# Optimization experiments

Hardware: AMD Instinct MI355X
Metric: run time of the kernel (lower is better)

The kernel has to match this reference:

```python
import jax, jax.numpy as jnp
import numpy as np
from jax import lax

NUM_HEADS = 8
NUM_LAYERS = 3


def _conv3d(x, w, b):
    # x: [B,C,D,H,W], w: [O,I,3,3,3] (torch Conv3d layout), padding=1, stride=1
    y = lax.conv_general_dilated(x, w, window_strides=(1, 1, 1),
                                 padding=[(1, 1)] * 3,
                                 dimension_numbers=('NCDHW', 'OIDHW', 'NCDHW'))
    return y + b[None, :, None, None, None]


def _attn(x, wq, bq, wk, bk, wv, bv, gamma):
    # Faithful translation of MultiHeadAttentionModule.forward
    B, C, D, H, W = x.shape
    N = D * H * W
    hd = C // NUM_HEADS
    scale = jnp.asarray(hd ** 0.5, x.dtype)
    xf = x.reshape(B, C, N).transpose(0, 2, 1)  # [B,N,C]

    def proj(wm, bm):
        # torch Linear: y = x @ W.T + b ; split C -> (heads, head_dim)
        return (xf @ wm.T + bm).reshape(B, N, NUM_HEADS, hd).transpose(0, 2, 1, 3)

    q = proj(wq, bq)  # [B,h,N,d]
    k = proj(wk, bk)
    v = proj(wv, bv)
    energy = jnp.einsum('bhnd,bhmd->bhnm', q, k) / scale  # [B,h,N,N]
    attn = jax.nn.softmax(energy, axis=-1)
    o = jnp.einsum('bhnm,bhmd->bhnd', attn, v)  # [B,h,N,d]
    # permute(0,1,3,2).view(in_shape): channel order is (head, head_dim)
    o = o.transpose(0, 1, 3, 2).reshape(B, C, D, H, W)
    return gamma * o + x


def setup_inputs() -> dict:
    key = jax.random.key(0)
    ks = jax.random.split(key, 16)
    B, Cin, D, H, W = 1, 64, 16, 16, 16
    Co = 128
    L = NUM_LAYERS
    s = 0.02
    return {
        'x': jax.random.normal(ks[0], (B, Cin, D, H, W), jnp.float32),
        'lateral_w': jax.random.normal(ks[1], (Co, Cin, 3, 3, 3), jnp.float32) * s,
        'lateral_b': jax.random.normal(ks[2], (Co,), jnp.float32) * s,
        'pos': jax.random.normal(ks[3], (1, Co, D, H, W), jnp.float32) * s,
        'qw': jax.random.normal(ks[4], (L, Co, Co), jnp.float32) * s,
        'qb': jax.random.normal(ks[5], (L, Co), jnp.float32) * s,
        'kw': jax.random.normal(ks[6], (L, Co, Co), jnp.float32) * s,
        'kb': jax.random.normal(ks[7], (L, Co), jnp.float32) * s,
        'vw': jax.random.normal(ks[8], (L, Co, Co), jnp.float32) * s,
        'vb': jax.random.normal(ks[9], (L, Co), jnp.float32) * s,
        'gamma': jnp.full((L,), 0.5, jnp.float32),
        'out_w': jax.random.normal(ks[10], (Co, Co, 3, 3, 3), jnp.float32) * s,  # ConvTranspose3d weight [in,out,k,k,k]
        'out_b': jax.random.normal(ks[11], (Co,), jnp.float32) * s,
    }


def reference(x, lateral_w, lateral_b, pos, qw, qb, kw, kb, vw, vb, gamma, out_w, out_b):
    # t_dim == 1 branch of FPN3DWithMultiHeadAttention.forward
    lat = _conv3d(x, lateral_w, lateral_b) + pos
    for i in range(NUM_LAYERS):
        lat = _attn(lat, qw[i], qb[i], kw[i], kb[i], vw[i], vb[i], gamma[i])
    # ConvTranspose3d(k=3, stride=1, pad=1) == Conv3d with spatially flipped,
    # channel-transposed kernel and padding k-1-p = 1
    w_eq = jnp.flip(out_w, axis=(2, 3, 4)).transpose(1, 0, 2, 3, 4)
    return _conv3d(lat, w_eq, out_b)
```

## Files before the change

### kernel.cpp

```cpp
#include <hip/hip_runtime.h>
#include <hip/hip_bf16.h>

#define NVOX 4096
#define CDIM 128

typedef __attribute__((ext_vector_type(8)))  short bf16x8;
typedef __attribute__((ext_vector_type(4)))  float f32x4;
typedef __attribute__((ext_vector_type(16))) float f32x16;

static __device__ __forceinline__ short f2bf(float f) {
    __hip_bfloat16 h = __float2bfloat16(f);
    union { __hip_bfloat16 h; short s; } u; u.h = h; return u.s;
}
static __device__ __forceinline__ float bf2f(short s) {
    union { unsigned u; float f; } u;
    u.u = ((unsigned)(unsigned short)s) << 16;
    return u.f;
}
static __device__ __forceinline__ float fexp2(float x) {
    return __builtin_amdgcn_exp2f(x);
}
__device__ __forceinline__ int permpos(int ci) {
    return (((ci >> 2) & 3) << 3) + (ci & 3) + ((ci & 16) >> 2) + ((ci >> 5) << 5);
}
__device__ __forceinline__ int invp(int p) {
    const int c = p >> 5, r = p & 31, g = (r >> 3) & 3, j = r & 7;
    return (c << 5) + (j < 4 ? (g << 2) + j : 16 + (g << 2) + (j - 4));
}
__device__ __forceinline__ int pos16(int d) {
    return (d & 3) | ((d & 4) << 1) | ((d & 8) >> 1);
}

__global__ __launch_bounds__(256) void pack_all(
    const float* __restrict__ x,  const float* __restrict__ lw,
    const float* __restrict__ qw, const float* __restrict__ kw, const float* __restrict__ vw,
    const float* __restrict__ ow,
    short* __restrict__ xp, short* __restrict__ wb1, short* __restrict__ wqkv, short* __restrict__ wb2,
    short* __restrict__ xp2)
{
    const int b = blockIdx.x;
    const int tid = threadIdx.x;
    if (b < 1458) {
        const int e = b * 256 + tid;
        if (e >= 5832 * 64) return;
        const int vp = e >> 6, p = e & 63;
        const int z = vp / 324, rem = vp - z * 324, y = rem / 18, xx = rem % 18;
        short val = 0;
        if (z >= 1 && z <= 16 && y >= 1 && y <= 16 && xx >= 1 && xx <= 16) {
            const int n = ((z - 1) * 16 + (y - 1)) * 16 + (xx - 1);
            val = f2bf(x[invp(p) * NVOX + n]);
        }
        xp[e] = val;
    } else if (b < 1458 + 864) {
        const int e = (b - 1458) * 256 + tid;
        if (e >= 27 * 128 * 64) return;
        const int t = e >> 13, co = (e >> 6) & 127, p = e & 63;
        wb1[e] = f2bf(lw[(co * 64 + invp(p)) * 27 + t]);
    } else if (b < 1458 + 864 + 576) {
        const int e = (b - 2322) * 256 + tid;
        if (e >= 3 * 3 * 128 * 128) return;
        const int l = e / 49152, r = e - l * 49152;
        const int m = r >> 14, co = (r >> 7) & 127, p = r & 127;
        const float* W = (m == 0 ? qw : m == 1 ? kw : vw) + l * 16384;
        wqkv[e] = f2bf(W[co * 128 + invp(p)]);
    } else if (b < 1458 + 864 + 576 + 1728) {
        const int e = (b - 2898) * 256 + tid;
        if (e >= 27 * 128 * 128) return;
        const int t = e >> 14, co = (e >> 7) & 127, p = e & 127;
        wb2[e] = f2bf(ow[(invp(p) * 128 + co) * 27 + (26 - t)]);
    } else {
        const int e = (b - 4626) * 256 + tid;
        if (e >= 5832 * 16) return;
        const int4 z4 = {0, 0, 0, 0};
        *reinterpret_cast<int4*>(xp2 + e * 8) = z4;
    }
}

__global__ __launch_bounds__(256) void conv1_mfma(
    const short* __restrict__ xp,
    const short* __restrict__ wb,
    const float* __restrict__ bias, const float* __restrict__ pos,
    short* __restrict__ latbf)
{
    __shared__ short bl[324 * 72];
    const int tid = threadIdx.x;
    const int g = blockIdx.x;
    const int cot = g >> 6;
    const int vgrp = g & 63;
    const int r0 = vgrp * 4;
    const int z = r0 >> 4, y0 = r0 & 15;

    for (int i = tid; i < 2592; i += 256) {
        const int col = i >> 3, pc = i & 7;
        const int line = col / 18, xq = col - line * 18;
        const int dz = line / 6, yi = line - dz * 6;
        const int4 v = *reinterpret_cast<const int4*>(
            xp + (((z + dz) * 18 + (y0 + yi)) * 18 + xq) * 64 + pc * 8);
        const int slot = ((((pc >> 2) ^ col) & 1) << 5) + ((pc & 3) << 3);
        *reinterpret_cast<int4*>(&bl[col * 72 + slot]) = v;
    }
    __syncthreads();

    const int wid = tid >> 6, lane = tid & 63;
    const int lg = lane >> 4, lq = lane & 15;
    const int wc = wid >> 1, wv = wid & 1;
    const int co0 = cot * 32 + wc * 16;

    const short* pA = wb + (co0 + lq) * 64 + lg * 8;

    auto ldA = [&](int t, bf16x8* A) {
        const short* p = pA + t * 8192;
        #pragma unroll
        for (int c = 0; c < 2; ++c) A[c] = *reinterpret_cast<const bf16x8*>(p + c * 32);
    };

    f32x4 acc0 = {0.f,0.f,0.f,0.f}, acc1 = {0.f,0.f,0.f,0.f};

    auto comp = [&](int t, const bf16x8* A) {
        const int dz = t / 9, r9 = t - dz * 9, dy = r9 / 3, dx = r9 - dy * 3;
        #pragma unroll
        for (int ry = 0; ry < 2; ++ry) {
            const int col = (dz * 6 + wv * 2 + ry + dy) * 18 + dx + lq;
            const short* bp = &bl[col * 72 + (lg << 3)];
            #pragma unroll
            for (int c = 0; c < 2; ++c) {
                const bf16x8 b = *reinterpret_cast<const bf16x8*>(bp + (((c ^ col) & 1) << 5));
                if (ry == 0) acc0 = __builtin_amdgcn_mfma_f32_16x16x32_bf16(A[c], b, acc0, 0, 0, 0);
                else         acc1 = __builtin_amdgcn_mfma_f32_16x16x32_bf16(A[c], b, acc1, 0, 0, 0);
            }
        }
    };

    bf16x8 A0[2], A1[2];
    int t = 0;
    ldA(0, A0);
    while (true) {
        if (t + 1 < 27) ldA(t + 1, A1);
        comp(t, A0);
        if (++t >= 27) break;
        if (t + 1 < 27) ldA(t + 1, A0);
        comp(t, A1);
        if (++t >= 27) break;
    }

    #pragma unroll
    for (int ry = 0; ry < 2; ++ry) {
        const f32x4 a = ry ? acc1 : acc0;
        const int n = (r0 + wv * 2 + ry) * 16 + lq;
        short4 s4;
        #pragma unroll
        for (int i = 0; i < 4; ++i) {
            const int co = co0 + 4 * lg + i;
            const float v = a[i] + bias[co] + pos[co * NVOX + n];
            ((short*)&s4)[i] = f2bf(v);
        }
        *reinterpret_cast<short4*>(latbf + n * 128 + permpos(co0 + 4 * lg)) = s4;
    }
}

__global__ __launch_bounds__(256) void proj_mfma(
    const short* __restrict__ latbf,
    const short* __restrict__ wl,
    const float* __restrict__ bq, const float* __restrict__ bk, const float* __restrict__ bv,
    short* __restrict__ qP, short* __restrict__ kP, short* __restrict__ vP)
{
    const int m = blockIdx.z;
    const int wid = threadIdx.x >> 6, lane = threadIdx.x & 63;
    const int lg = lane >> 4, lq = lane & 15;
    const int co0 = blockIdx.y * 16;
    const int row0 = (blockIdx.x * 4 + wid) * 2;

    const short* A = wl + m * 16384 + (co0 + lq) * 128 + lg * 8;
    bf16x8 Af[4];
    #pragma unroll
    for (int c = 0; c < 4; ++c) Af[c] = *reinterpret_cast<const bf16x8*>(A + c * 32);

    const short* Bp0 = latbf + (row0 * 16 + lq) * 128 + lg * 8;
    const short* Bp1 = Bp0 + 16 * 128;
    bf16x8 Bf0[4], Bf1[4];
    #pragma unroll
    for (int c = 0; c < 4; ++c) Bf0[c] = *reinterpret_cast<const bf16x8*>(Bp0 + c * 32);
    #pragma unroll
    for (int c = 0; c < 4; ++c) Bf1[c] = *reinterpret_cast<const bf16x8*>(Bp1 + c * 32);

    f32x4 a0a = {0.f,0.f,0.f,0.f}, a0b = a0a, a1a = a0a, a1b = a0a;
    a0a = __builtin_amdgcn_mfma_f32_16x16x32_bf16(Af[0], Bf0[0], a0a, 0, 0, 0);
    a1a = __builtin_amdgcn_mfma_f32_16x16x32_bf16(Af[0], Bf1[0], a1a, 0, 0, 0);
    a0b = __builtin_amdgcn_mfma_f32_16x16x32_bf16(Af[1], Bf0[1], a0b, 0, 0, 0);
    a1b = __builtin_amdgcn_mfma_f32_16x16x32_bf16(Af[1], Bf1[1], a1b, 0, 0, 0);
    a0a = __builtin_amdgcn_mfma_f32_16x16x32_bf16(Af[2], Bf0[2], a0a, 0, 0, 0);
    a1a = __builtin_amdgcn_mfma_f32_16x16x32_bf16(Af[2], Bf1[2], a1a, 0, 0, 0);
    a0b = __builtin_amdgcn_mfma_f32_16x16x32_bf16(Af[3], Bf0[3], a0b, 0, 0, 0);
    a1b = __builtin_amdgcn_mfma_f32_16x16x32_bf16(Af[3], Bf1[3], a1b, 0, 0, 0);

    const int h = blockIdx.y;
    #pragma unroll
    for (int rr = 0; rr < 2; ++rr) {
        const f32x4 acc = rr ? (a1a + a1b) : (a0a + a0b);
        const int row = row0 + rr;
        const int n = row * 16 + lq;
        if (m == 2) {
            const int col = row * 16 + pos16(lq);
            #pragma unroll
            for (int r = 0; r < 4; ++r) {
                const int d = lg * 4 + r;
                vP[(h * 17 + d) * NVOX + col] = f2bf(acc[r] + bv[co0 + d]);
            }
            if (lg == 0) vP[(h * 17 + 16) * NVOX + col] = (short)0x3F80;
        } else {
            const float* bias = (m == 0) ? bq : bk;
            const float S = (m == 0) ? 0.25f * 1.4426950408889634f : 1.f;
            const int pg = ((lg & 1) << 3) | ((lg & 2) << 1);
            short4 s4;
            #pragma unroll
            for (int r = 0; r < 4; ++r) {
                const int co = co0 + lg * 4 + r;
                ((short*)&s4)[r] = f2bf((acc[r] + bias[co]) * S);
            }
            short* dst = (m == 0) ? qP : kP;
            *reinterpret_cast<short4*>(dst + ((h << 12) + n) * 16 + pg) = s4;
        }
    }
}

__global__ __launch_bounds__(512) void attn_mfma(
    const short* __restrict__ qP, const short* __restrict__ kP, const short* __restrict__ vP,
    short* __restrict__ latbf, short* __restrict__ outbf,
    const float* __restrict__ gamma, int layer, int last)
{
    __shared__ float smO[8][64][17];
    const int tid = threadIdx.x;
    const int wid = tid >> 6, lane = tid & 63;
    const int l5 = lane >> 5, lm = lane & 31;
    const int qg = wid >> 2, ksp = wid & 3;
    const int h = blockIdx.y;
    const int qbase = blockIdx.x * 128 + qg * 64;

    const bf16x8 qf0 = *reinterpret_cast<const bf16x8*>(
        qP + (((h << 12) + qbase + lm) << 4) + l5 * 8);
    const bf16x8 qf1 = *reinterpret_cast<const bf16x8*>(
        qP + (((h << 12) + qbase + 32 + lm) << 4) + l5 * 8);

    const short* kbase = kP + (((size_t)h) << 16);
    const int vrow = (lm & 16) ? 16 : lm;
    const short* vbase = vP + ((size_t)h * 17 + vrow) * NVOX + l5 * 8;

    f32x16 acc0 = {0.f,0.f,0.f,0.f,0.f,0.f,0.f,0.f,0.f,0.f,0.f,0.f,0.f,0.f,0.f,0.f};
    f32x16 acc1 = acc0;
    const f32x16 zero = acc0;

    bf16x8 kfA, v0A, v1A, kfB, v0B, v1B;
    auto LD = [&](int kc, bf16x8& kf, bf16x8& v0, bf16x8& v1) {
        kf = *reinterpret_cast<const bf16x8*>(kbase + ((kc + lm) << 4) + l5 * 8);
        v0 = *reinterpret_cast<const bf16x8*>(vbase + kc);
        v1 = *reinterpret_cast<const bf16x8*>(vbase + kc + 16);
    };
    auto COMP = [&](const bf16x8& kf, const bf16x8& v0, const bf16x8& v1) {
        const f32x16 S0 = __builtin_amdgcn_mfma_f32_32x32x16_bf16(kf, qf0, zero, 0, 0, 0);
        const f32x16 S1 = __builtin_amdgcn_mfma_f32_32x32x16_bf16(kf, qf1, zero, 0, 0, 0);
        short p0[16], p1[16];
        #pragma unroll
        for (int r = 0; r < 16; ++r) p0[r] = f2bf(fexp2(S0[r]));
        #pragma unroll
        for (int r = 0; r < 16; ++r) p1[r] = f2bf(fexp2(S1[r]));
        const bf16x8 pa00 = {p0[0],p0[1],p0[2],p0[3],p0[4],p0[5],p0[6],p0[7]};
        const bf16x8 pa01 = {p0[8],p0[9],p0[10],p0[11],p0[12],p0[13],p0[14],p0[15]};
        const bf16x8 pa10 = {p1[0],p1[1],p1[2],p1[3],p1[4],p1[5],p1[6],p1[7]};
        const bf16x8 pa11 = {p1[8],p1[9],p1[10],p1[11],p1[12],p1[13],p1[14],p1[15]};
        acc0 = __builtin_amdgcn_mfma_f32_32x32x16_bf16(pa00, v0, acc0, 0, 0, 0);
        acc0 = __builtin_amdgcn_mfma_f32_32x32x16_bf16(pa01, v1, acc0, 0, 0, 0);
        acc1 = __builtin_amdgcn_mfma_f32_32x32x16_bf16(pa10, v0, acc1, 0, 0, 0);
        acc1 = __builtin_amdgcn_mfma_f32_32x32x16_bf16(pa11, v1, acc1, 0, 0, 0);
    };

    int kc = ksp * 1024;
    int it = 0;
    LD(kc, kfA, v0A, v1A);
    while (true) {
        if (it + 1 < 32) LD(kc + 32, kfB, v0B, v1B);
        COMP(kfA, v0A, v1A);
        kc += 32;
        if (++it >= 32) break;
        if (it + 1 < 32) LD(kc + 32, kfA, v0A, v1A);
        COMP(kfB, v0B, v1B);
        kc += 32;
        if (++it >= 32) break;
    }

    if (lm <= 16) {
        #pragma unroll
        for (int r = 0; r < 16; ++r) {
            const int qrow = (r & 3) + 8 * (r >> 2) + 4 * l5;
            smO[wid][qrow][lm]      = acc0[r];
            smO[wid][32 + qrow][lm] = acc1[r];
        }
    }
    __syncthreads();

    const int q = tid >> 2;
    const int d0 = (tid & 3) * 4;
    const int g4 = (q >> 6) * 4, ql = q & 63;
    const float ls = smO[g4][ql][16] + smO[g4+1][ql][16] + smO[g4+2][ql][16] + smO[g4+3][ql][16];
    const float ginv = gamma[layer] / ls;
    const int n = blockIdx.x * 128 + q;
    const int c0 = (h << 4) + d0;
    const short4 r4 = *reinterpret_cast<const short4*>(latbf + n * 128 + permpos(c0));
    short4 s4;
    #pragma unroll
    for (int dd = 0; dd < 4; ++dd) {
        const int d = d0 + dd;
        const float Ov = smO[g4][ql][d] + smO[g4+1][ql][d] + smO[g4+2][ql][d] + smO[g4+3][ql][d];
        const float val = Ov * ginv + bf2f(((const short*)&r4)[dd]);
        ((short*)&s4)[dd] = f2bf(val);
    }
    if (!last) {
        *reinterpret_cast<short4*>(latbf + n * 128 + permpos(c0)) = s4;
    } else {
        const int zq = n >> 8, yq = (n >> 4) & 15, xq = n & 15;
        const int vp = (zq + 1) * 324 + (yq + 1) * 18 + (xq + 1);
        *reinterpret_cast<short4*>(outbf + vp * 128 + permpos(c0)) = s4;
    }
}

__global__ __launch_bounds__(256) void conv2_mfma(
    const short* __restrict__ xp,
    const short* __restrict__ wb,
    const float* __restrict__ bias,
    float* __restrict__ out)
{
    __shared__ short bl[324 * 136];
    const int tid = threadIdx.x;
    const int g = blockIdx.x;
    const int cot = g >> 6;
    const int vgrp = g & 63;
    const int r0 = vgrp * 4;
    const int z = r0 >> 4, y0 = r0 & 15;

    for (int i = tid; i < 5184; i += 256) {
        const int col = i >> 4, pc = i & 15;
        const int line = col / 18, xq = col - line * 18;
        const int dz = line / 6, yi = line - dz * 6;
        const int4 v = *reinterpret_cast<const int4*>(
            xp + (((z + dz) * 18 + (y0 + yi)) * 18 + xq) * 128 + pc * 8);
        const int slot = ((((pc >> 2) ^ col) & 3) << 5) + ((pc & 3) << 3);
        *reinterpret_cast<int4*>(&bl[col * 136 + slot]) = v;
    }
    __syncthreads();

    const int wid = tid >> 6, lane = tid & 63;
    const int lg = lane >> 4, lq = lane & 15;
    const int wc = wid >> 1, wv = wid & 1;
    const int co0 = cot * 32 + wc * 16;

    const short* pA = wb + (co0 + lq) * 128 + lg * 8;

    auto ldA = [&](int t, bf16x8* A) {
        const short* p = pA + t * 16384;
        #pragma unroll
        for (int c = 0; c < 4; ++c) A[c] = *reinterpret_cast<const bf16x8*>(p + c * 32);
    };

    f32x4 acc0 = {0.f,0.f,0.f,0.f}, acc1 = {0.f,0.f,0.f,0.f};

    auto comp = [&](int t, const bf16x8* A) {
        const int dz = t / 9, r9 = t - dz * 9, dy = r9 / 3, dx = r9 - dy * 3;
        #pragma unroll
        for (int ry = 0; ry < 2; ++ry) {
            const int col = (dz * 6 + wv * 2 + ry + dy) * 18 + dx + lq;
            const short* bp = &bl[col * 136 + (lg << 3)];
            #pragma unroll
            for (int c = 0; c < 4; ++c) {
                const bf16x8 b = *reinterpret_cast<const bf16x8*>(bp + (((c ^ col) & 3) << 5));
                if (ry == 0) acc0 = __builtin_amdgcn_mfma_f32_16x16x32_bf16(A[c], b, acc0, 0, 0, 0);
                else         acc1 = __builtin_amdgcn_mfma_f32_16x16x32_bf16(A[c], b, acc1, 0, 0, 0);
            }
        }
    };

    bf16x8 A0[4], A1[4];
    int t = 0;
    ldA(0, A0);
    while (true) {
        if (t + 1 < 27) ldA(t + 1, A1);
        comp(t, A0);
        if (++t >= 27) break;
        if (t + 1 < 27) ldA(t + 1, A0);
        comp(t, A1);
        if (++t >= 27) break;
    }

    #pragma unroll
    for (int ry = 0; ry < 2; ++ry) {
        const f32x4 a = ry ? acc1 : acc0;
        const int n = (r0 + wv * 2 + ry) * 16 + lq;
        #pragma unroll
        for (int i = 0; i < 4; ++i) {
            const int co = co0 + 4 * lg + i;
            out[co * NVOX + n] = a[i] + bias[co];
        }
    }
}

extern "C" void kernel_launch(void* const* d_in, const int* in_sizes, int n_in,
                              void* d_out, int out_size, void* d_ws, size_t ws_size,
                              hipStream_t stream) {
    const float* x     = (const float*)d_in[0];
    const float* lw    = (const float*)d_in[1];
    const float* lb    = (const float*)d_in[2];
    const float* pos   = (const float*)d_in[3];
    const float* qw    = (const float*)d_in[4];
    const float* qb    = (const float*)d_in[5];
    const float* kw    = (const float*)d_in[6];
    const float* kb    = (const float*)d_in[7];
    const float* vw    = (const float*)d_in[8];
    const float* vb    = (const float*)d_in[9];
    const float* gamma = (const float*)d_in[10];
    const float* ow    = (const float*)d_in[11];
    const float* ob    = (const float*)d_in[12];

    short* latbf = (short*)d_ws;
    short* qP    = latbf + 524288;
    short* kP    = qP + 524288;
    short* vP    = kP + 524288;
    short* xpad  = vP + 557056;
    short* xpad2 = xpad + 373248;
    short* wbf1  = xpad2 + 746496;
    short* wqkv  = wbf1 + 221184;
    short* wbf2  = wqkv + 442368;

    pack_all<<<4809, 256, 0, stream>>>(x, lw, qw, kw, vw, ow, xpad, wbf1, wqkv, wbf2, xpad2);

    conv1_mfma<<<256, 256, 0, stream>>>(xpad, wbf1, lb, pos, latbf);

    for (int i = 0; i < 3; ++i) {
        const int last = (i == 2);
        proj_mfma<<<dim3(32, 8, 3), 256, 0, stream>>>(
            latbf, wqkv + i * 49152, qb + i * 128, kb + i * 128, vb + i * 128, qP, kP, vP);
        attn_mfma<<<dim3(32, 8), 512, 0, stream>>>(
            qP, kP, vP, latbf, last ? xpad2 : latbf, gamma, i, last);
    }

    conv2_mfma<<<256, 256, 0, stream>>>(xpad2, wbf2, ob, (float*)d_out);
}
```

Before: 125.9 us.

## Coalesce weight/input packing via LDS transposes and use cheap bf16 rounding in attention

The packing kernel is restructured so that each block stages a tile of the input or of a weight tensor in shared memory and then writes the permuted bf16 layout. This replaces scattered per-element gathers with coalesced reads, and the grid shrinks from 4809 to 684 blocks. The conv2 weight packing now scatters through permpos instead of gathering through invp. Separately, the exp-to-bf16 conversion in the attention inner loop uses a simple add-and-shift round, which drops the NaN handling and round-to-even of the library conversion to save ALU work in the hot loop.

```diff
diff --git a/kernel.cpp b/kernel.cpp
--- a/kernel.cpp
+++ b/kernel.cpp
@@ -11,6 +11,10 @@
 static __device__ __forceinline__ short f2bf(float f) {
     __hip_bfloat16 h = __float2bfloat16(f);
     union { __hip_bfloat16 h; short s; } u; u.h = h; return u.s;
+}
+static __device__ __forceinline__ short f2bf_r(float f) {
+    union { float f; unsigned u; } v; v.f = f;
+    return (short)((v.u + 0x8000u) >> 16);
 }
 static __device__ __forceinline__ float bf2f(short s) {
     union { unsigned u; float f; } u;
@@ -38,38 +42,77 @@
     short* __restrict__ xp, short* __restrict__ wb1, short* __restrict__ wqkv, short* __restrict__ wb2,
     short* __restrict__ xp2)
 {
+    __shared__ __align__(16) char sm[27904];
     const int b = blockIdx.x;
     const int tid = threadIdx.x;
-    if (b < 1458) {
-        const int e = b * 256 + tid;
-        if (e >= 5832 * 64) return;
-        const int vp = e >> 6, p = e & 63;
+
+    if (b < 64) {
+        float* lds = (float*)sm;
+        const int n0 = b * 64;
+        for (int i = tid; i < 4096; i += 256) {
+            const int c = i >> 6, nl = i & 63;
+            lds[nl * 65 + c] = x[c * NVOX + n0 + nl];
+        }
+        __syncthreads();
+        for (int i = tid; i < 4096; i += 256) {
+            const int nl = i >> 6, p = i & 63;
+            const int n = n0 + nl;
+            const int z = n >> 8, y = (n >> 4) & 15, xx = n & 15;
+            const int vp = (z + 1) * 324 + (y + 1) * 18 + (xx + 1);
+            xp[vp * 64 + p] = f2bf(lds[nl * 65 + invp(p)]);
+        }
+    } else if (b < 87) {
+        const int vp = (b - 64) * 256 + tid;
+        if (vp >= 5832) return;
         const int z = vp / 324, rem = vp - z * 324, y = rem / 18, xx = rem % 18;
-        short val = 0;
-        if (z >= 1 && z <= 16 && y >= 1 && y <= 16 && xx >= 1 && xx <= 16) {
-            const int n = ((z - 1) * 16 + (y - 1)) * 16 + (xx - 1);
-            val = f2bf(x[invp(p) * NVOX + n]);
-        }
-        xp[e] = val;
-    } else if (b < 1458 + 864) {
-        const int e = (b - 1458) * 256 + tid;
-        if (e >= 27 * 128 * 64) return;
-        const int t = e >> 13, co = (e >> 6) & 127, p = e & 63;
-        wb1[e] = f2bf(lw[(co * 64 + invp(p)) * 27 + t]);
-    } else if (b < 1458 + 864 + 576) {
-        const int e = (b - 2322) * 256 + tid;
-        if (e >= 3 * 3 * 128 * 128) return;
-        const int l = e / 49152, r = e - l * 49152;
-        const int m = r >> 14, co = (r >> 7) & 127, p = r & 127;
+        if (z >= 1 && z <= 16 && y >= 1 && y <= 16 && xx >= 1 && xx <= 16) return;
+        const int4 z4 = {0, 0, 0, 0};
+        int4* dst = (int4*)(xp + vp * 64);
+        #pragma unroll
+        for (int j = 0; j < 8; ++j) dst[j] = z4;
+    } else if (b < 215) {
+        float* lds = (float*)sm;
+        const int co = b - 87;
+        for (int i = tid; i < 1728; i += 256) lds[i] = lw[co * 1728 + i];
+        __syncthreads();
+        for (int i = tid; i < 1728; i += 256) {
+            const int t = i >> 6, p = i & 63;
+            wb1[t * 8192 + co * 64 + p] = f2bf(lds[invp(p) * 27 + t]);
+        }
+    } else if (b < 287) {
+        float* lds = (float*)sm;
+        const int u = b - 215;
+        const int l = u / 24, rm = u - l * 24;
+        const int m = rm >> 3, cg = rm & 7;
+        const int co0 = cg * 16;
         const float* W = (m == 0 ? qw : m == 1 ? kw : vw) + l * 16384;
-        wqkv[e] = f2bf(W[co * 128 + invp(p)]);
-    } else if (b < 1458 + 864 + 576 + 1728) {
-        const int e = (b - 2898) * 256 + tid;
-        if (e >= 27 * 128 * 128) return;
-        const int t = e >> 14, co = (e >> 7) & 127, p = e & 127;
-        wb2[e] = f2bf(ow[(invp(p) * 128 + co) * 27 + (26 - t)]);
+        for (int i = tid; i < 2048; i += 256) {
+            const int co_l = i >> 7, ci = i & 127;
+            lds[i] = W[(co0 + co_l) * 128 + ci];
+        }
+        __syncthreads();
+        for (int i = tid; i < 2048; i += 256) {
+            const int co_l = i >> 7, p = i & 127;
+            wqkv[((l * 3 + m) * 128 + co0 + co_l) * 128 + p] = f2bf(lds[co_l * 128 + invp(p)]);
+        }
+    } else if (b < 319) {
+        short* sld = (short*)sm;
+        const int u = b - 287;
+        const int ci_g = u >> 2, co_g = u & 3;
+        const int ci0 = ci_g * 16, co0 = co_g * 32;
+        for (int i = tid; i < 13824; i += 256) {
+            const int ci_l = i / 864, r = i - ci_l * 864;
+            sld[ci_l * 872 + r] = f2bf(ow[(ci0 + ci_l) * 3456 + co0 * 27 + r]);
+        }
+        __syncthreads();
+        for (int i = tid; i < 13824; i += 256) {
+            const int t = i >> 9, r2 = i & 511;
+            const int co_l = r2 >> 4, ci_l = r2 & 15;
+            wb2[t * 16384 + (co0 + co_l) * 128 + permpos(ci0 + ci_l)] =
+                sld[ci_l * 872 + co_l * 27 + (26 - t)];
+        }
     } else {
-        const int e = (b - 4626) * 256 + tid;
+        const int e = (b - 319) * 256 + tid;
         if (e >= 5832 * 16) return;
         const int4 z4 = {0, 0, 0, 0};
         *reinterpret_cast<int4*>(xp2 + e * 8) = z4;
@@ -260,9 +303,9 @@
         const f32x16 S1 = __builtin_amdgcn_mfma_f32_32x32x16_bf16(kf, qf1, zero, 0, 0, 0);
         short p0[16], p1[16];
         #pragma unroll
-        for (int r = 0; r < 16; ++r) p0[r] = f2bf(fexp2(S0[r]));
-        #pragma unroll
-        for (int r = 0; r < 16; ++r) p1[r] = f2bf(fexp2(S1[r]));
+        for (int r = 0; r < 16; ++r) p0[r] = f2bf_r(fexp2(S0[r]));
+        #pragma unroll
+        for (int r = 0; r < 16; ++r) p1[r] = f2bf_r(fexp2(S1[r]));
         const bf16x8 pa00 = {p0[0],p0[1],p0[2],p0[3],p0[4],p0[5],p0[6],p0[7]};
         const bf16x8 pa01 = {p0[8],p0[9],p0[10],p0[11],p0[12],p0[13],p0[14],p0[15]};
         const bf16x8 pa10 = {p1[0],p1[1],p1[2],p1[3],p1[4],p1[5],p1[6],p1[7]};
@@ -428,7 +471,7 @@
     short* wqkv  = wbf1 + 221184;
     short* wbf2  = wqkv + 442368;
 
-    pack_all<<<4809, 256, 0, stream>>>(x, lw, qw, kw, vw, ow, xpad, wbf1, wqkv, wbf2, xpad2);
+    pack_all<<<684, 256, 0, stream>>>(x, lw, qw, kw, vw, ow, xpad, wbf1, wqkv, wbf2, xpad2);
 
     conv1_mfma<<<256, 256, 0, stream>>>(xpad, wbf1, lb, pos, latbf);
 
```

Result: slower. 141.6 us (+12.5%).
